# Kernel optimization log

Measured on AMD Instinct MI355X. Metric: run time of the kernel, lower is better.

Reference implementation:

```python
import jax, jax.numpy as jnp
import numpy as np

PARTS = [[0, 1, 2, 3, 4], [5, 7, 9], [6, 8, 10], [11, 13, 15], [12, 14, 16]]
# joint i -> index of first part containing i (matches get_corr_joints)
JOINTS = np.array([0, 0, 0, 0, 0, 1, 2, 1, 2, 1, 2, 3, 4, 3, 4, 3, 4])
P = len(PARTS)
EPS = 1e-5


def _bn(y, g, b, m, v):
    # eval-mode BatchNorm2d over channel axis=1 of NCHW-like tensor
    scale = g / jnp.sqrt(v + EPS)
    return y * scale[None, :, None, None] + (b - m * scale)[None, :, None, None]


def setup_inputs() -> dict:
    C, Cq = 256, 64
    N, T, V = 64, 300, 17
    key = jax.random.key(0)
    ks = jax.random.split(key, 20)
    u = lambda k, s: jax.random.uniform(k, s, jnp.float32, 0.5, 1.5)
    n = lambda k, s: jax.random.normal(k, s, jnp.float32) * 0.1
    return {
        "x": jax.random.normal(ks[0], (N, C, T, V), jnp.float32),
        "part_w": n(ks[1], (P, Cq, C)),
        "part_b": n(ks[2], (P, Cq)),
        "pbn_g": u(ks[3], (P, Cq)),
        "pbn_b": n(ks[4], (P, Cq)),
        "pbn_m": n(ks[5], (P, Cq)),
        "pbn_v": u(ks[6], (P, Cq)),
        "fc1_w": n(ks[7], (Cq, Cq)),
        "fc1_b": n(ks[8], (Cq,)),
        "fbn_g": u(ks[9], (Cq,)),
        "fbn_b": n(ks[10], (Cq,)),
        "fbn_m": n(ks[11], (Cq,)),
        "fbn_v": u(ks[12], (Cq,)),
        "fc2_w": n(ks[13], (C * P, Cq)),
        "fc2_b": n(ks[14], (C * P,)),
        "bn_g": u(ks[15], (C,)),
        "bn_b": n(ks[16], (C,)),
        "bn_m": n(ks[17], (C,)),
        "bn_v": u(ks[18], (C,)),
    }


def reference(x, part_w, part_b, pbn_g, pbn_b, pbn_m, pbn_v,
              fc1_w, fc1_b, fbn_g, fbn_b, fbn_m, fbn_v,
              fc2_w, fc2_b, bn_g, bn_b, bn_m, bn_v):
    N, C, T, V = x.shape
    # per-part 1x1 conv + BN + ReLU + global average pool -> [N, Cq], summed over parts
    pooled = 0.0
    for p, idx in enumerate(PARTS):
        xp = x[:, :, :, np.array(idx)]                       # [N, C, T, k]
        y = jnp.einsum('nctv,qc->nqtv', xp, part_w[p]) + part_b[p][None, :, None, None]
        y = jax.nn.relu(_bn(y, pbn_g[p], pbn_b[p], pbn_m[p], pbn_v[p]))
        pooled = pooled + y.mean(axis=(2, 3))                # [N, Cq]
    # fcn: 1x1 conv + BN + ReLU + 1x1 conv (acting on [N, Cq, 1, 1])
    h = pooled @ fc1_w.T + fc1_b
    scale = fbn_g / jnp.sqrt(fbn_v + EPS)
    h = jax.nn.relu(h * scale + (fbn_b - fbn_m * scale))
    z = h @ fc2_w.T + fc2_b                                  # [N, C*P]
    att = jax.nn.softmax(z.reshape(N, C, P), axis=-1)        # [N, C, P]
    # gather attention per joint, broadcast over time
    att_v = att[:, :, JOINTS]                                # [N, C, V]
    out = x * att_v[:, :, None, :]
    return jax.nn.relu(_bn(out, bn_g, bn_b, bn_m, bn_v) + x)
```

## Files before the change

kernel.cpp:

```cpp
#include <hip/hip_runtime.h>
#include <hip/hip_bf16.h>


typedef __attribute__((ext_vector_type(8))) short short8;
typedef __attribute__((ext_vector_type(4))) float f32x4;
typedef float f4u __attribute__((ext_vector_type(4), aligned(4)));

__device__ __forceinline__ unsigned short f2bf(float f) {
    unsigned int u = __float_as_uint(f);
    u = (u + 0x7FFFu + ((u >> 16) & 1u)) >> 16;
    return (unsigned short)u;
}

__global__ void fold_kernel(
    const float* __restrict__ part_b, const float* __restrict__ pbn_g,
    const float* __restrict__ pbn_b,  const float* __restrict__ pbn_m,
    const float* __restrict__ pbn_v,
    const float* __restrict__ fc1_b,  const float* __restrict__ fbn_g,
    const float* __restrict__ fbn_b,  const float* __restrict__ fbn_m,
    const float* __restrict__ fbn_v,
    const float* __restrict__ bn_g,   const float* __restrict__ bn_b,
    const float* __restrict__ bn_m,   const float* __restrict__ bn_v,
    float* __restrict__ ps, float* __restrict__ pb,
    float* __restrict__ fs, float* __restrict__ fb,
    float* __restrict__ cs, float* __restrict__ cb)
{
    int tid = threadIdx.x;
    if (tid < 320) {
        float s = pbn_g[tid] * rsqrtf(pbn_v[tid] + 1e-5f);
        ps[tid] = s;
        pb[tid] = part_b[tid] * s + pbn_b[tid] - pbn_m[tid] * s;
    }
    if (tid < 64) {
        float s = fbn_g[tid] * rsqrtf(fbn_v[tid] + 1e-5f);
        fs[tid] = s;
        fb[tid] = fc1_b[tid] * s + fbn_b[tid] - fbn_m[tid] * s;
    }
    if (tid < 256) {
        float s = bn_g[tid] * rsqrtf(bn_v[tid] + 1e-5f);
        cs[tid] = s;
        cb[tid] = bn_b[tid] - bn_m[tid] * s;
    }
}

__global__ void conv_w_kernel(const float* __restrict__ pw, unsigned short* __restrict__ wq)
{
    int i = blockIdx.x * 256 + threadIdx.x;
    if (i < 5 * 64 * 256) wq[i] = f2bf(pw[i]);
}

__global__ __launch_bounds__(256) void part_pool_kernel(
    const float* __restrict__ x, const unsigned short* __restrict__ wq,
    const float* __restrict__ ps, const float* __restrict__ pb,
    float* __restrict__ pooled)
{
    constexpr int ROWC[17] = {0,1,2,3,4, 80,128, 81,129, 82,130, 176,224, 177,225, 178,226};
    constexpr int CNTV[17] = {5,5,5,5,5, 3,3,3,3,3,3, 3,3,3,3,3,3};
    constexpr int PMAP[17] = {0,0,0,0,0, 1,1,1, 2,2,2, 3,3,3, 4,4,4};
    constexpr int BASE[5]  = {0,80,128,176,224};
    constexpr int CNT[5]   = {5,3,3,3,3};
    constexpr float COEF[5] = {1.f/1500.f, 1.f/900.f, 1.f/900.f, 1.f/900.f, 1.f/900.f};

    __shared__ short Xs[272 * 64];

    const int blk = blockIdx.x;
    const int n   = blk / 19;
    const int tb  = (blk % 19) * 16;
    const int tid = threadIdx.x;
    const int lane = tid & 63;
    const int wv   = tid >> 6;
    const int r15  = lane & 15;
    const int g    = lane >> 4;
    const int key  = (r15 & 7) << 4;

    const int cp  = tid & 31;
    const int oct = tid >> 5;

    f32x4 acc[17];
    #pragma unroll
    for (int m = 0; m < 17; ++m) acc[m] = (f32x4){0.f, 0.f, 0.f, 0.f};

    for (int cc = 0; cc < 256; cc += 64) {
        __syncthreads();
        #pragma unroll
        for (int dt = 0; dt < 2; ++dt) {
            const int tl = 2 * oct + dt;
            const int tg = tb + tl;
            float r0[17], r1[17];
            if (tg < 300) {
                const float* g0 = x + ((size_t)(n * 256 + cc + 2 * cp) * 300 + tg) * 17;
                const float* g1 = g0 + 300 * 17;
                f4u a0 = *(const f4u*)(g0);     f4u b0 = *(const f4u*)(g1);
                f4u a1 = *(const f4u*)(g0 + 4); f4u b1 = *(const f4u*)(g1 + 4);
                f4u a2 = *(const f4u*)(g0 + 8); f4u b2 = *(const f4u*)(g1 + 8);
                f4u a3 = *(const f4u*)(g0 +12); f4u b3 = *(const f4u*)(g1 +12);
                #pragma unroll
                for (int j = 0; j < 4; ++j) {
                    r0[j]    = a0[j]; r1[j]    = b0[j];
                    r0[4+j]  = a1[j]; r1[4+j]  = b1[j];
                    r0[8+j]  = a2[j]; r1[8+j]  = b2[j];
                    r0[12+j] = a3[j]; r1[12+j] = b3[j];
                }
                r0[16] = g0[16]; r1[16] = g1[16];
            } else {
                #pragma unroll
                for (int v = 0; v < 17; ++v) { r0[v] = 0.f; r1[v] = 0.f; }
            }
            #pragma unroll
            for (int v = 0; v < 17; ++v) {
                const int row = ROWC[v] + tl * CNTV[v];
                unsigned int pk = (unsigned int)f2bf(r0[v]) | ((unsigned int)f2bf(r1[v]) << 16);
                const int off = row * 128 + ((cp * 4) ^ ((row & 7) << 4));
                *(unsigned int*)((char*)Xs + off) = pk;
            }
        }
        __syncthreads();

        #pragma unroll
        for (int kk = 0; kk < 2; ++kk) {
            short8 bfr[5];
            #pragma unroll
            for (int p = 0; p < 5; ++p) {
                const int widx = ((p * 64 + wv * 16 + r15) << 8) + cc + kk * 32 + g * 8;
                bfr[p] = *(const short8*)(wq + widx);
            }
            const int cofs = ((kk * 64 + g * 16) ^ key);
            #pragma unroll
            for (int m = 0; m < 17; ++m) {
                short8 a = *(const short8*)((const char*)Xs + (m * 16 + r15) * 128 + cofs);
                acc[m] = __builtin_amdgcn_mfma_f32_16x16x32_bf16(a, bfr[PMAP[m]], acc[m], 0, 0, 0);
            }
        }
    }

    const int q = wv * 16 + r15;
    float s5[5], b5[5];
    #pragma unroll
    for (int p = 0; p < 5; ++p) { s5[p] = ps[(p << 6) + q]; b5[p] = pb[(p << 6) + q]; }

    float sum = 0.f;
    #pragma unroll
    for (int m = 0; m < 17; ++m) {
        const int p = PMAP[m];
        #pragma unroll
        for (int rg = 0; rg < 4; ++rg) {
            const int row = m * 16 + g * 4 + rg;
            const int tl  = (row - BASE[p]) / CNT[p];
            if (tb + tl < 300) {
                float y = fmaf(s5[p], acc[m][rg], b5[p]);
                sum = fmaf(fmaxf(y, 0.f), COEF[p], sum);
            }
        }
    }
    sum += __shfl_xor(sum, 16);
    sum += __shfl_xor(sum, 32);
    if (g == 0) atomicAdd(&pooled[(n << 6) + q], sum);
}

__global__ __launch_bounds__(256) void fc_att_kernel(
    const float* __restrict__ pooled, const float* __restrict__ fc1_w,
    const float* __restrict__ fs, const float* __restrict__ fb,
    const float* __restrict__ fc2_w, const float* __restrict__ fc2_b,
    float* __restrict__ att)
{
    __shared__ float pl[64];
    __shared__ float hl[64];
    const int n = blockIdx.x;
    const int tid = threadIdx.x;

    if (tid < 64) pl[tid] = pooled[(n << 6) + tid];
    __syncthreads();
    if (tid < 64) {
        float d = 0.f;
        #pragma unroll
        for (int j = 0; j < 64; ++j) d = fmaf(pl[j], fc1_w[(tid << 6) + j], d);
        hl[tid] = fmaxf(fmaf(d, fs[tid], fb[tid]), 0.f);
    }
    __syncthreads();

    const int c = tid;
    float z[5];
    #pragma unroll
    for (int p = 0; p < 5; ++p) {
        const float* wrow = fc2_w + ((size_t)(c * 5 + p) << 6);
        float d = fc2_b[c * 5 + p];
        #pragma unroll
        for (int i = 0; i < 64; ++i) d = fmaf(hl[i], wrow[i], d);
        z[p] = d;
    }
    float m = z[0];
    #pragma unroll
    for (int p = 1; p < 5; ++p) m = fmaxf(m, z[p]);
    float e[5], ssum = 0.f;
    #pragma unroll
    for (int p = 0; p < 5; ++p) { e[p] = __expf(z[p] - m); ssum += e[p]; }
    const float inv = 1.f / ssum;
    #pragma unroll
    for (int p = 0; p < 5; ++p)
        att[((size_t)((n << 8) + c)) * 5 + p] = e[p] * inv;
}

__global__ __launch_bounds__(256) void apply_att_kernel(
    const float* __restrict__ x, const float* __restrict__ att,
    const float* __restrict__ cs, const float* __restrict__ cb,
    float* __restrict__ out)
{
    __shared__ float mult[17];
    const int nc  = blockIdx.x;
    const int c   = nc & 255;
    const int tid = threadIdx.x;

    if (tid < 17) {
        const int v = tid;
        const int p = (v < 5) ? 0 : ((v < 11) ? (2 - (v & 1)) : (4 - (v & 1)));
        mult[v] = fmaf(att[(size_t)nc * 5 + p], cs[c], 1.0f);
    }
    __syncthreads();

    const float cbc = cb[c];
    const float4* xp = (const float4*)(x + (size_t)nc * 5100);
    float4* op = (float4*)(out + (size_t)nc * 5100);

    for (int f = tid; f < 1275; f += 256) {
        float4 xv = xp[f];
        const int v0 = (4 * f) % 17;
        float o[4];
        const float xi[4] = {xv.x, xv.y, xv.z, xv.w};
        #pragma unroll
        for (int j = 0; j < 4; ++j) {
            int vj = v0 + j; if (vj >= 17) vj -= 17;
            o[j] = fmaxf(fmaf(xi[j], mult[vj], cbc), 0.f);
        }
        float4 ov; ov.x = o[0]; ov.y = o[1]; ov.z = o[2]; ov.w = o[3];
        op[f] = ov;
    }
}

extern "C" void kernel_launch(void* const* d_in, const int* in_sizes, int n_in,
                              void* d_out, int out_size, void* d_ws, size_t ws_size,
                              hipStream_t stream)
{
    const float* x      = (const float*)d_in[0];
    const float* part_w = (const float*)d_in[1];
    const float* part_b = (const float*)d_in[2];
    const float* pbn_g  = (const float*)d_in[3];
    const float* pbn_b  = (const float*)d_in[4];
    const float* pbn_m  = (const float*)d_in[5];
    const float* pbn_v  = (const float*)d_in[6];
    const float* fc1_w  = (const float*)d_in[7];
    const float* fc1_b  = (const float*)d_in[8];
    const float* fbn_g  = (const float*)d_in[9];
    const float* fbn_b  = (const float*)d_in[10];
    const float* fbn_m  = (const float*)d_in[11];
    const float* fbn_v  = (const float*)d_in[12];
    const float* fc2_w  = (const float*)d_in[13];
    const float* fc2_b  = (const float*)d_in[14];
    const float* bn_g   = (const float*)d_in[15];
    const float* bn_b   = (const float*)d_in[16];
    const float* bn_m   = (const float*)d_in[17];
    const float* bn_v   = (const float*)d_in[18];

    float* ws     = (float*)d_ws;
    float* pooled = ws;
    float* att    = ws + 4096;
    float* ps     = ws + 86016;
    float* pbias  = ws + 86336;
    float* fs     = ws + 86656;
    float* fb     = ws + 86720;
    float* cs     = ws + 86784;
    float* cb     = ws + 87040;
    unsigned short* wq = (unsigned short*)(ws + 87296);

    hipMemsetAsync(pooled, 0, 4096 * sizeof(float), stream);

    fold_kernel<<<1, 320, 0, stream>>>(part_b, pbn_g, pbn_b, pbn_m, pbn_v,
                                       fc1_b, fbn_g, fbn_b, fbn_m, fbn_v,
                                       bn_g, bn_b, bn_m, bn_v,
                                       ps, pbias, fs, fb, cs, cb);
    conv_w_kernel<<<320, 256, 0, stream>>>(part_w, wq);
    part_pool_kernel<<<64 * 19, 256, 0, stream>>>(x, wq, ps, pbias, pooled);
    fc_att_kernel<<<64, 256, 0, stream>>>(pooled, fc1_w, fs, fb, fc2_w, fc2_b, att);
    apply_att_kernel<<<16384, 256, 0, stream>>>(x, att, cs, cb, (float*)d_out);
}
```

Baseline: 279.9 us.

## Switch part-pool GEMM to 32x32x16 MFMA tiles with per-wave row-tile split

Reworks the part-pooling kernel to use 32x32x16 bf16 MFMA with 16-wide accumulators. The shared X tile is padded so each part's rows fill whole 32-row tiles, and each wave now owns up to three row tiles across all 64 output channels, instead of every wave covering every row for 16 channels. Each wave loads weights for at most two parts, and padded rows are no longer zero-filled. The aim is fewer MFMA issues and weight loads per K step, and an occupancy hint of 3 blocks is added. The cost is a larger LDS footprint, uneven per-wave work, and more complex epilogue index math.

```diff
diff --git a/kernel.cpp b/kernel.cpp
--- a/kernel.cpp
+++ b/kernel.cpp
@@ -2,8 +2,8 @@
 #include <hip/hip_bf16.h>
 
 
-typedef __attribute__((ext_vector_type(8))) short short8;
-typedef __attribute__((ext_vector_type(4))) float f32x4;
+typedef __attribute__((ext_vector_type(8)))  short short8;
+typedef __attribute__((ext_vector_type(16))) float f32x16;
 typedef float f4u __attribute__((ext_vector_type(4), aligned(4)));
 
 __device__ __forceinline__ unsigned short f2bf(float f) {
@@ -49,36 +49,45 @@
     if (i < 5 * 64 * 256) wq[i] = f2bf(pw[i]);
 }
 
-__global__ __launch_bounds__(256) void part_pool_kernel(
+__global__ __launch_bounds__(256, 3) void part_pool_kernel(
     const float* __restrict__ x, const unsigned short* __restrict__ wq,
-    const float* __restrict__ ps, const float* __restrict__ pb,
+    const float* __restrict__ ps, const float* __restrict__ pbs,
     float* __restrict__ pooled)
 {
-    constexpr int ROWC[17] = {0,1,2,3,4, 80,128, 81,129, 82,130, 176,224, 177,225, 178,226};
+    constexpr int ROWC[17] = {0,1,2,3,4, 96,160, 97,161, 98,162, 224,288, 225,289, 226,290};
     constexpr int CNTV[17] = {5,5,5,5,5, 3,3,3,3,3,3, 3,3,3,3,3,3};
-    constexpr int PMAP[17] = {0,0,0,0,0, 1,1,1, 2,2,2, 3,3,3, 4,4,4};
-    constexpr int BASE[5]  = {0,80,128,176,224};
-    constexpr int CNT[5]   = {5,3,3,3,3};
-    constexpr float COEF[5] = {1.f/1500.f, 1.f/900.f, 1.f/900.f, 1.f/900.f, 1.f/900.f};
-
-    __shared__ short Xs[272 * 64];
-
-    const int blk = blockIdx.x;
-    const int n   = blk / 19;
-    const int tb  = (blk % 19) * 16;
-    const int tid = threadIdx.x;
+
+    __shared__ short Xs[352 * 64];
+
+    const int blk  = blockIdx.x;
+    const int n    = blk / 19;
+    const int tb   = (blk % 19) * 16;
+    const int tid  = threadIdx.x;
     const int lane = tid & 63;
     const int wv   = tid >> 6;
-    const int r15  = lane & 15;
-    const int g    = lane >> 4;
-    const int key  = (r15 & 7) << 4;
+    const int l31  = lane & 31;
+    const int hi   = lane >> 5;
+    const int key  = (l31 & 7) << 4;
+
+    const int t0 = wv * 3, t1 = wv * 3 + 1, t2k = wv * 3 + 2;
+    const bool has2 = (t2k < 11);
+    auto PART = [](int t) { return (t < 3) ? 0 : (((t - 3) >> 1) + 1); };
+    const int P0 = PART(t0), P1 = PART(t1), P2 = has2 ? PART(t2k) : P1;
+    const int pa  = P0;
+    const int pbp = (P2 != P0) ? P2 : ((P1 != P0) ? P1 : P0);
+    const bool s1 = (P1 != pa);
+    const bool s2 = (P2 != pa);
 
     const int cp  = tid & 31;
     const int oct = tid >> 5;
 
-    f32x4 acc[17];
-    #pragma unroll
-    for (int m = 0; m < 17; ++m) acc[m] = (f32x4){0.f, 0.f, 0.f, 0.f};
+    f32x16 acc[3][2];
+    #pragma unroll
+    for (int i = 0; i < 3; ++i)
+        #pragma unroll
+        for (int qt = 0; qt < 2; ++qt)
+            #pragma unroll
+            for (int r = 0; r < 16; ++r) acc[i][qt][r] = 0.f;
 
     for (int cc = 0; cc < 256; cc += 64) {
         __syncthreads();
@@ -86,10 +95,10 @@
         for (int dt = 0; dt < 2; ++dt) {
             const int tl = 2 * oct + dt;
             const int tg = tb + tl;
-            float r0[17], r1[17];
             if (tg < 300) {
                 const float* g0 = x + ((size_t)(n * 256 + cc + 2 * cp) * 300 + tg) * 17;
                 const float* g1 = g0 + 300 * 17;
+                float r0[17], r1[17];
                 f4u a0 = *(const f4u*)(g0);     f4u b0 = *(const f4u*)(g1);
                 f4u a1 = *(const f4u*)(g0 + 4); f4u b1 = *(const f4u*)(g1 + 4);
                 f4u a2 = *(const f4u*)(g0 + 8); f4u b2 = *(const f4u*)(g1 + 8);
@@ -102,59 +111,77 @@
                     r0[12+j] = a3[j]; r1[12+j] = b3[j];
                 }
                 r0[16] = g0[16]; r1[16] = g1[16];
-            } else {
                 #pragma unroll
-                for (int v = 0; v < 17; ++v) { r0[v] = 0.f; r1[v] = 0.f; }
-            }
-            #pragma unroll
-            for (int v = 0; v < 17; ++v) {
-                const int row = ROWC[v] + tl * CNTV[v];
-                unsigned int pk = (unsigned int)f2bf(r0[v]) | ((unsigned int)f2bf(r1[v]) << 16);
-                const int off = row * 128 + ((cp * 4) ^ ((row & 7) << 4));
-                *(unsigned int*)((char*)Xs + off) = pk;
+                for (int v = 0; v < 17; ++v) {
+                    const int row = ROWC[v] + tl * CNTV[v];
+                    unsigned int pk = (unsigned int)f2bf(r0[v]) | ((unsigned int)f2bf(r1[v]) << 16);
+                    const int off = row * 128 + ((cp * 4) ^ ((row & 7) << 4));
+                    *(unsigned int*)((char*)Xs + off) = pk;
+                }
             }
         }
         __syncthreads();
 
         #pragma unroll
-        for (int kk = 0; kk < 2; ++kk) {
-            short8 bfr[5];
-            #pragma unroll
-            for (int p = 0; p < 5; ++p) {
-                const int widx = ((p * 64 + wv * 16 + r15) << 8) + cc + kk * 32 + g * 8;
-                bfr[p] = *(const short8*)(wq + widx);
+        for (int kk = 0; kk < 4; ++kk) {
+            const int kbase = cc + kk * 16 + hi * 8;
+            short8 Ba0 = *(const short8*)(wq + ((pa  * 64      + l31) << 8) + kbase);
+            short8 Ba1 = *(const short8*)(wq + ((pa  * 64 + 32 + l31) << 8) + kbase);
+            short8 Bb0 = Ba0, Bb1 = Ba1;
+            if (pbp != pa) {
+                Bb0 = *(const short8*)(wq + ((pbp * 64      + l31) << 8) + kbase);
+                Bb1 = *(const short8*)(wq + ((pbp * 64 + 32 + l31) << 8) + kbase);
             }
-            const int cofs = ((kk * 64 + g * 16) ^ key);
-            #pragma unroll
-            for (int m = 0; m < 17; ++m) {
-                short8 a = *(const short8*)((const char*)Xs + (m * 16 + r15) * 128 + cofs);
-                acc[m] = __builtin_amdgcn_mfma_f32_16x16x32_bf16(a, bfr[PMAP[m]], acc[m], 0, 0, 0);
+            const int coff = kk * 32 + hi * 16;
+
+            short8 A0 = *(const short8*)((const char*)Xs + (t0  * 32 + l31) * 128 + (coff ^ key));
+            acc[0][0] = __builtin_amdgcn_mfma_f32_32x32x16_bf16(A0, Ba0, acc[0][0], 0, 0, 0);
+            acc[0][1] = __builtin_amdgcn_mfma_f32_32x32x16_bf16(A0, Ba1, acc[0][1], 0, 0, 0);
+
+            short8 A1 = *(const short8*)((const char*)Xs + (t1  * 32 + l31) * 128 + (coff ^ key));
+            acc[1][0] = __builtin_amdgcn_mfma_f32_32x32x16_bf16(A1, s1 ? Bb0 : Ba0, acc[1][0], 0, 0, 0);
+            acc[1][1] = __builtin_amdgcn_mfma_f32_32x32x16_bf16(A1, s1 ? Bb1 : Ba1, acc[1][1], 0, 0, 0);
+
+            if (has2) {
+                short8 A2 = *(const short8*)((const char*)Xs + (t2k * 32 + l31) * 128 + (coff ^ key));
+                acc[2][0] = __builtin_amdgcn_mfma_f32_32x32x16_bf16(A2, s2 ? Bb0 : Ba0, acc[2][0], 0, 0, 0);
+                acc[2][1] = __builtin_amdgcn_mfma_f32_32x32x16_bf16(A2, s2 ? Bb1 : Ba1, acc[2][1], 0, 0, 0);
             }
         }
     }
 
-    const int q = wv * 16 + r15;
-    float s5[5], b5[5];
-    #pragma unroll
-    for (int p = 0; p < 5; ++p) { s5[p] = ps[(p << 6) + q]; b5[p] = pb[(p << 6) + q]; }
-
-    float sum = 0.f;
-    #pragma unroll
-    for (int m = 0; m < 17; ++m) {
-        const int p = PMAP[m];
-        #pragma unroll
-        for (int rg = 0; rg < 4; ++rg) {
-            const int row = m * 16 + g * 4 + rg;
-            const int tl  = (row - BASE[p]) / CNT[p];
-            if (tb + tl < 300) {
-                float y = fmaf(s5[p], acc[m][rg], b5[p]);
-                sum = fmaf(fmaxf(y, 0.f), COEF[p], sum);
+    float sq0 = 0.f, sq1 = 0.f;
+    #pragma unroll
+    for (int i = 0; i < 3; ++i) {
+        if (i == 2 && !has2) break;
+        const int tI   = wv * 3 + i;
+        const int Pi   = (i == 0) ? P0 : (i == 1 ? P1 : P2);
+        const int tip  = (tI < 3) ? tI : ((tI - 3) & 1);
+        const int RPp  = (Pi == 0) ? 80 : 48;
+        const float mulc = (Pi == 0) ? 0.200000003f : 0.333333343f;
+        const float coef = (Pi == 0) ? (1.f / 1500.f) : (1.f / 900.f);
+        const float sA = ps [Pi * 64      + l31];
+        const float bA = pbs[Pi * 64      + l31];
+        const float sB = ps [Pi * 64 + 32 + l31];
+        const float bB = pbs[Pi * 64 + 32 + l31];
+        #pragma unroll
+        for (int r = 0; r < 16; ++r) {
+            const int rit = (r & 3) + ((r >> 2) << 3) + (hi << 2);
+            const int rip = tip * 32 + rit;
+            const int tl  = (int)((float)rip * mulc);
+            if (rip < RPp && tb + tl < 300) {
+                const float y0 = fmaf(sA, acc[i][0][r], bA);
+                sq0 = fmaf(fmaxf(y0, 0.f), coef, sq0);
+                const float y1 = fmaf(sB, acc[i][1][r], bB);
+                sq1 = fmaf(fmaxf(y1, 0.f), coef, sq1);
             }
         }
     }
-    sum += __shfl_xor(sum, 16);
-    sum += __shfl_xor(sum, 32);
-    if (g == 0) atomicAdd(&pooled[(n << 6) + q], sum);
+    sq0 += __shfl_xor(sq0, 32);
+    sq1 += __shfl_xor(sq1, 32);
+    const int   qq  = (lane < 32) ? l31 : (32 + l31);
+    const float val = (lane < 32) ? sq0 : sq1;
+    atomicAdd(&pooled[(n << 6) + qq], val);
 }
 
 __global__ __launch_bounds__(256) void fc_att_kernel(
```

New measurement: 342.3 us. +22.3%, slower.

## Coalesce x loads in part-pool via two-stage LDS transpose and pre-swizzled weights

Applied to the files above, without the earlier changes.

The part-pool kernel now loads x as contiguous float4 runs along the flattened (t,v) axis, so global reads are fully coalesced. The bf16 data goes into a staging LDS buffer, then a second LDS pass interleaves channel pairs into a swizzled row-major tile keyed by a precomputed joint-to-row table. Weights are pre-permuted into MFMA fragment order so each B load is one contiguous short8. The K chunk shrinks to 32 channels, with launch bounds set to 3 blocks per CU. This trades an extra LDS round trip and twice as many barriers for better global memory efficiency and occupancy.

```diff
diff --git a/kernel.cpp b/kernel.cpp
--- a/kernel.cpp
+++ b/kernel.cpp
@@ -43,100 +43,140 @@
     }
 }
 
-__global__ void conv_w_kernel(const float* __restrict__ pw, unsigned short* __restrict__ wq)
+__global__ void conv_w_kernel(const float* __restrict__ pw, unsigned short* __restrict__ wq2)
 {
     int i = blockIdx.x * 256 + threadIdx.x;
-    if (i < 5 * 64 * 256) wq[i] = f2bf(pw[i]);
-}
-
-__global__ __launch_bounds__(256) void part_pool_kernel(
-    const float* __restrict__ x, const unsigned short* __restrict__ wq,
-    const float* __restrict__ ps, const float* __restrict__ pb,
+    if (i < 5 * 64 * 256) {
+        int p = i >> 14;
+        int q = (i >> 8) & 63;
+        int c = i & 255;
+        int kc = c >> 5, g = (c >> 3) & 3, j = c & 7;
+        int wv = q >> 4, r15 = q & 15;
+        wq2[((((p * 8 + kc) * 4 + wv) * 4 + g) * 16 + r15) * 8 + j] = f2bf(pw[i]);
+    }
+}
+
+__global__ __launch_bounds__(256, 3) void part_pool_kernel(
+    const float* __restrict__ x, const unsigned short* __restrict__ wq2,
+    const float* __restrict__ ps, const float* __restrict__ pbs,
     float* __restrict__ pooled)
 {
-    constexpr int ROWC[17] = {0,1,2,3,4, 80,128, 81,129, 82,130, 176,224, 177,225, 178,226};
-    constexpr int CNTV[17] = {5,5,5,5,5, 3,3,3,3,3,3, 3,3,3,3,3,3};
     constexpr int PMAP[17] = {0,0,0,0,0, 1,1,1, 2,2,2, 3,3,3, 4,4,4};
     constexpr int BASE[5]  = {0,80,128,176,224};
     constexpr int CNT[5]   = {5,3,3,3,3};
     constexpr float COEF[5] = {1.f/1500.f, 1.f/900.f, 1.f/900.f, 1.f/900.f, 1.f/900.f};
 
-    __shared__ short Xs[272 * 64];
-
-    const int blk = blockIdx.x;
-    const int n   = blk / 19;
-    const int tb  = (blk % 19) * 16;
-    const int tid = threadIdx.x;
+    __shared__ short Xn[32 * 272];
+    __shared__ short Xt[272 * 32];
+    __shared__ unsigned short rows4[68][4];
+
+    const int tid  = threadIdx.x;
     const int lane = tid & 63;
     const int wv   = tid >> 6;
     const int r15  = lane & 15;
     const int g    = lane >> 4;
-    const int key  = (r15 & 7) << 4;
-
-    const int cp  = tid & 31;
-    const int oct = tid >> 5;
+
+    const int blk = blockIdx.x;
+    const int n   = blk / 19;
+    const int tb  = (blk % 19) * 16;
+    const bool tail = (tb + 16 > 300);
+
+    if (tid < 68) {
+        #pragma unroll
+        for (int j = 0; j < 4; ++j) {
+            const int f = 4 * tid + j;
+            const int t = (int)(((unsigned)f * 61681u) >> 20);
+            const int v = f - 17 * t;
+            int row;
+            if (v < 5)        row = v + 5 * t;
+            else if (v < 11)  row = ((v & 1) ? (80 + ((v - 5) >> 1)) : (128 + ((v - 6) >> 1))) + 3 * t;
+            else              row = ((v & 1) ? (176 + ((v - 11) >> 1)) : (224 + ((v - 12) >> 1))) + 3 * t;
+            rows4[tid][j] = (unsigned short)row;
+        }
+    }
 
     f32x4 acc[17];
     #pragma unroll
     for (int m = 0; m < 17; ++m) acc[m] = (f32x4){0.f, 0.f, 0.f, 0.f};
 
-    for (int cc = 0; cc < 256; cc += 64) {
+    const size_t xbase = (size_t)n * 1305600 + (size_t)tb * 17;
+
+    for (int cc = 0; cc < 256; cc += 32) {
         __syncthreads();
-        #pragma unroll
-        for (int dt = 0; dt < 2; ++dt) {
-            const int tl = 2 * oct + dt;
-            const int tg = tb + tl;
-            float r0[17], r1[17];
-            if (tg < 300) {
-                const float* g0 = x + ((size_t)(n * 256 + cc + 2 * cp) * 300 + tg) * 17;
-                const float* g1 = g0 + 300 * 17;
-                f4u a0 = *(const f4u*)(g0);     f4u b0 = *(const f4u*)(g1);
-                f4u a1 = *(const f4u*)(g0 + 4); f4u b1 = *(const f4u*)(g1 + 4);
-                f4u a2 = *(const f4u*)(g0 + 8); f4u b2 = *(const f4u*)(g1 + 8);
-                f4u a3 = *(const f4u*)(g0 +12); f4u b3 = *(const f4u*)(g1 +12);
+
+        #pragma unroll
+        for (int it = 0; it < 9; ++it) {
+            const int pi = it * 256 + tid;
+            if (pi < 2176) {
+                const int c = (int)(((unsigned)pi * 61681u) >> 22);
+                const int q = pi - 68 * c;
+                const float* gp = x + xbase + (size_t)(cc + c) * 5100 + 4 * q;
+                unsigned int lo, hi2;
+                if (!tail) {
+                    f4u xv = *(const f4u*)gp;
+                    lo  = (unsigned int)f2bf(xv[0]) | ((unsigned int)f2bf(xv[1]) << 16);
+                    hi2 = (unsigned int)f2bf(xv[2]) | ((unsigned int)f2bf(xv[3]) << 16);
+                } else {
+                    float e[4];
+                    #pragma unroll
+                    for (int j = 0; j < 4; ++j) {
+                        const int f = 4 * q + j;
+                        const int t = (int)(((unsigned)f * 61681u) >> 20);
+                        e[j] = 0.f;
+                        if (tb + t < 300) e[j] = gp[j];
+                    }
+                    lo  = (unsigned int)f2bf(e[0]) | ((unsigned int)f2bf(e[1]) << 16);
+                    hi2 = (unsigned int)f2bf(e[2]) | ((unsigned int)f2bf(e[3]) << 16);
+                }
+                *(uint2*)&Xn[c * 272 + 4 * q] = make_uint2(lo, hi2);
+            }
+        }
+        __syncthreads();
+
+        #pragma unroll
+        for (int it = 0; it < 5; ++it) {
+            const int pi = it * 256 + tid;
+            if (pi < 1088) {
+                const int cp = (int)(((unsigned)pi * 61681u) >> 22);
+                const int q  = pi - 68 * cp;
+                const uint2 a = *(const uint2*)&Xn[(2 * cp)     * 272 + 4 * q];
+                const uint2 b = *(const uint2*)&Xn[(2 * cp + 1) * 272 + 4 * q];
+                unsigned int w[4];
+                w[0] = (a.x & 0xFFFFu) | (b.x << 16);
+                w[1] = (a.x >> 16)     | (b.x & 0xFFFF0000u);
+                w[2] = (a.y & 0xFFFFu) | (b.y << 16);
+                w[3] = (a.y >> 16)     | (b.y & 0xFFFF0000u);
+                const ushort4 rq = *(const ushort4*)&rows4[q][0];
+                const int rr[4] = {rq.x, rq.y, rq.z, rq.w};
                 #pragma unroll
                 for (int j = 0; j < 4; ++j) {
-                    r0[j]    = a0[j]; r1[j]    = b0[j];
-                    r0[4+j]  = a1[j]; r1[4+j]  = b1[j];
-                    r0[8+j]  = a2[j]; r1[8+j]  = b2[j];
-                    r0[12+j] = a3[j]; r1[12+j] = b3[j];
+                    const int row = rr[j];
+                    const int off = row * 64 + ((cp * 4) ^ (((row >> 1) & 3) << 4));
+                    *(unsigned int*)((char*)Xt + off) = w[j];
                 }
-                r0[16] = g0[16]; r1[16] = g1[16];
-            } else {
-                #pragma unroll
-                for (int v = 0; v < 17; ++v) { r0[v] = 0.f; r1[v] = 0.f; }
             }
-            #pragma unroll
-            for (int v = 0; v < 17; ++v) {
-                const int row = ROWC[v] + tl * CNTV[v];
-                unsigned int pk = (unsigned int)f2bf(r0[v]) | ((unsigned int)f2bf(r1[v]) << 16);
-                const int off = row * 128 + ((cp * 4) ^ ((row & 7) << 4));
-                *(unsigned int*)((char*)Xs + off) = pk;
-            }
         }
         __syncthreads();
 
-        #pragma unroll
-        for (int kk = 0; kk < 2; ++kk) {
-            short8 bfr[5];
-            #pragma unroll
-            for (int p = 0; p < 5; ++p) {
-                const int widx = ((p * 64 + wv * 16 + r15) << 8) + cc + kk * 32 + g * 8;
-                bfr[p] = *(const short8*)(wq + widx);
-            }
-            const int cofs = ((kk * 64 + g * 16) ^ key);
-            #pragma unroll
-            for (int m = 0; m < 17; ++m) {
-                short8 a = *(const short8*)((const char*)Xs + (m * 16 + r15) * 128 + cofs);
-                acc[m] = __builtin_amdgcn_mfma_f32_16x16x32_bf16(a, bfr[PMAP[m]], acc[m], 0, 0, 0);
-            }
+        const int kc = cc >> 5;
+        short8 bfr[5];
+        #pragma unroll
+        for (int p = 0; p < 5; ++p)
+            bfr[p] = *(const short8*)(wq2 + ((((p * 8 + kc) * 4 + wv) * 4 + g) * 16 + r15) * 8);
+
+        #pragma unroll
+        for (int m = 0; m < 17; ++m) {
+            const int row = m * 16 + r15;
+            const int off = row * 64 + ((g * 16) ^ (((row >> 1) & 3) << 4));
+            short8 A = *(const short8*)((const char*)Xt + off);
+            acc[m] = __builtin_amdgcn_mfma_f32_16x16x32_bf16(A, bfr[PMAP[m]], acc[m], 0, 0, 0);
         }
     }
 
     const int q = wv * 16 + r15;
     float s5[5], b5[5];
     #pragma unroll
-    for (int p = 0; p < 5; ++p) { s5[p] = ps[(p << 6) + q]; b5[p] = pb[(p << 6) + q]; }
+    for (int p = 0; p < 5; ++p) { s5[p] = ps[(p << 6) + q]; b5[p] = pbs[(p << 6) + q]; }
 
     float sum = 0.f;
     #pragma unroll
@@ -269,7 +309,7 @@
     float* fb     = ws + 86720;
     float* cs     = ws + 86784;
     float* cb     = ws + 87040;
-    unsigned short* wq = (unsigned short*)(ws + 87296);
+    unsigned short* wq2 = (unsigned short*)(ws + 87296);
 
     hipMemsetAsync(pooled, 0, 4096 * sizeof(float), stream);
 
@@ -277,8 +317,8 @@
                                        fc1_b, fbn_g, fbn_b, fbn_m, fbn_v,
                                        bn_g, bn_b, bn_m, bn_v,
                                        ps, pbias, fs, fb, cs, cb);
-    conv_w_kernel<<<320, 256, 0, stream>>>(part_w, wq);
-    part_pool_kernel<<<64 * 19, 256, 0, stream>>>(x, wq, ps, pbias, pooled);
+    conv_w_kernel<<<320, 256, 0, stream>>>(part_w, wq2);
+    part_pool_kernel<<<64 * 19, 256, 0, stream>>>(x, wq2, ps, pbias, pooled);
     fc_att_kernel<<<64, 256, 0, stream>>>(pooled, fc1_w, fs, fb, fc2_w, fc2_b, att);
     apply_att_kernel<<<16384, 256, 0, stream>>>(x, att, cs, cb, (float*)d_out);
 }
```

Measured after the change: 285.7 us. 1.02x slower.
